# Kernel tuning notes

Measured on AMD Instinct MI355X. Metric: run time of the kernel, lower is better.

Reference implementation:

```python
import jax, jax.numpy as jnp
import numpy as np

GAMMA = 0.3          # surrogate gradient scale (LinearSpikeMC.gamma)
K = 2                # num_channels: multi-compartment count
T = 3                # timesteps
B = 4                # batch
LABELS = 10
CONV_CFG = [64, 64, 128, 128, 256, 256, 256, 512, 512, 512, 512, 512, 512]
POOL_AFTER = {1, 3, 6, 9}  # avg-pool after these conv indices (VGG16 'A' positions)


@jax.custom_vjp
def spike_mc(even, odd):
    # one-hot multi-compartment spike: fire where even>0 AND odd>=0
    return jnp.where((even > 0.0) & (odd >= 0.0), 1.0, 0.0).astype(even.dtype)

def _spike_fwd(even, odd):
    return spike_mc(even, odd), (even, odd)

def _spike_bwd(res, g):
    even, odd = res
    ge = GAMMA * jnp.maximum(1.0 - jnp.abs(even), 0.0) * g
    go = -GAMMA * jnp.maximum(1.0 - jnp.abs(odd), 0.0) * g
    # torch backward loop never writes the last odd compartment's grad
    go = go.at[-1].set(0.0)
    return ge, go

spike_mc.defvjp(_spike_fwd, _spike_bwd)


def conv3x3(x, w):
    return jax.lax.conv_general_dilated(
        x, w, (1, 1), 'SAME', dimension_numbers=('NCHW', 'OIHW', 'NCHW'))


def avgpool2(x):
    b, c, h, w = x.shape
    return x.reshape(b, c, h // 2, 2, w // 2, 2).mean(axis=(3, 5))


def lif(mem, syn, thr, leak):
    # leaky integrate; compartment i fires when 2^i*thr < mem <= 2^{i+1}*thr
    mem = leak * mem + syn
    pw = (2.0 ** jnp.arange(K, dtype=mem.dtype)).reshape((K,) + (1,) * mem.ndim)
    even = mem[None] / (pw * thr) - 1.0
    odd = 1.0 - mem[None] / (2.0 * pw * thr)
    sp = spike_mc(even, odd)            # [K, ...] one-hot spikes
    val = jnp.sum(pw * sp, axis=0)      # decoded value sum_i 2^i * s_i
    mem = mem - thr * val               # soft reset (reset_to_zero=0)
    return mem, val


def setup_inputs():
    key = jax.random.key(0)
    ks = jax.random.split(key, 32)
    inp = {"x": jax.random.normal(ks[0], (B, 3, 32, 32), jnp.float32)}
    in_c = 3
    for i, out_c in enumerate(CONV_CFG):
        std = float(np.sqrt(2.0 / (9.0 * out_c)))  # kaiming init from _initialize_weights2
        inp[f"w{i}"] = jax.random.normal(ks[1 + i], (out_c, in_c, 3, 3), jnp.float32) * std
        in_c = out_c
    inp["fc0"] = jax.random.normal(ks[20], (4096, 512 * 2 * 2), jnp.float32) * 0.01
    inp["fc1"] = jax.random.normal(ks[21], (4096, 4096), jnp.float32) * 0.01
    inp["fc2"] = jax.random.normal(ks[22], (LABELS, 4096), jnp.float32) * 0.01
    inp["thr"] = jnp.ones((15,), jnp.float32)   # per-layer thresholds
    inp["leak"] = jnp.ones((15,), jnp.float32)  # per-layer leaks
    return inp


def reference(x, w0, w1, w2, w3, w4, w5, w6, w7, w8, w9, w10, w11, w12,
              fc0, fc1, fc2, thr, leak):
    conv_ws = [w0, w1, w2, w3, w4, w5, w6, w7, w8, w9, w10, w11, w12]
    b = x.shape[0]
    # membranes sized at each conv's output resolution (neuron_init)
    mems = []
    s = 32
    for i, c in enumerate(CONV_CFG):
        mems.append(jnp.zeros((b, c, s, s), x.dtype))
        if i in POOL_AFTER:
            s //= 2
    carry0 = (tuple(mems),
              jnp.zeros((b, 4096), x.dtype),
              jnp.zeros((b, 4096), x.dtype),
              jnp.zeros((b, fc2.shape[0]), x.dtype))

    def step(carry, _):
        mems_c, m0, m1, logits = carry
        out = x  # analog input each timestep (input_encoding=1)
        new = []
        for i in range(13):
            m, out = lif(mems_c[i], conv3x3(out, conv_ws[i]), thr[i], leak[i])
            new.append(m)
            if i in POOL_AFTER:
                out = avgpool2(out)
        out = out.reshape(b, -1)
        m0, out = lif(m0, out @ fc0.T, thr[13], leak[13])
        m1, out = lif(m1, out @ fc1.T, thr[14], leak[14])
        logits = logits + out @ fc2.T  # final linear accumulates, no spiking
        return (tuple(new), m0, m1, logits), None

    carry, _ = jax.lax.scan(step, carry0, None, length=T)
    return carry[3]
```

## Files before the change

kernel.cpp:

```cpp
#include <hip/hip_runtime.h>


#define BATCH 4

__device__ __forceinline__ float lif_update(float mem_in, float syn, float thr,
                                            float leak, float* mem_out) {
    float m = leak * mem_in + syn;
    float val = 0.f;
    if ((m / thr - 1.f > 0.f) && (1.f - m / (2.f * thr) >= 0.f)) val += 1.f;
    if ((m / (2.f * thr) - 1.f > 0.f) && (1.f - m / (4.f * thr) >= 0.f)) val += 2.f;
    *mem_out = m - thr * val;
    return val;
}

__global__ void conv_lif0_kernel(const float* __restrict__ in,
                                 const float* __restrict__ w,
                                 float* __restrict__ out0,
                                 float* __restrict__ out1,
                                 float* __restrict__ out2,
                                 const float* __restrict__ thr_v,
                                 const float* __restrict__ leak_v,
                                 int IC, int OC, int H, int W, int n) {
    int idx = blockIdx.x * blockDim.x + threadIdx.x;
    if (idx >= n) return;
    int x  = idx % W;
    int y  = (idx / W) % H;
    int oc = (idx / (W * H)) % OC;
    int b  = idx / (W * H * OC);

    const float* wp = w + (size_t)oc * IC * 9;
    const float* ip = in + (size_t)b * IC * H * W;

    float syn = 0.f;
    for (int ic = 0; ic < IC; ++ic) {
        const float* ipc = ip + (size_t)ic * H * W;
        const float* wpc = wp + ic * 9;
#pragma unroll
        for (int ky = 0; ky < 3; ++ky) {
            int yy = y + ky - 1;
            if (yy < 0 || yy >= H) continue;
#pragma unroll
            for (int kx = 0; kx < 3; ++kx) {
                int xx = x + kx - 1;
                if (xx < 0 || xx >= W) continue;
                syn = fmaf(ipc[yy * W + xx], wpc[ky * 3 + kx], syn);
            }
        }
    }
    float thr = thr_v[0], leak = leak_v[0];
    float m = 0.f;
    float v0 = lif_update(m, syn, thr, leak, &m);
    float v1 = lif_update(m, syn, thr, leak, &m);
    float v2 = lif_update(m, syn, thr, leak, &m);
    out0[idx] = v0;
    out1[idx] = v1;
    out2[idx] = v2;
}

__device__ __forceinline__ void mid_load(float v[9], const float* __restrict__ ip,
                                         const int off[9], const bool msk[9]) {
#pragma unroll
    for (int k = 0; k < 9; ++k) v[k] = msk[k] ? ip[off[k]] : 0.f;
}

template <int OCT>
__device__ __forceinline__ void mid_fma(const float v[9], const float* __restrict__ wp,
                                        int IC, float acc[OCT]) {
#pragma unroll
    for (int t = 0; t < OCT; ++t) {
        const float* wt = wp + (size_t)t * IC * 9;
#pragma unroll
        for (int k = 0; k < 9; ++k) acc[t] = fmaf(v[k], wt[k], acc[t]);
    }
}

template <int OCT, int NW, int POOL>
__global__ __launch_bounds__(NW * 64)
void conv_mid3_kernel(const float* __restrict__ in0,
                      const float* __restrict__ in1,
                      const float* __restrict__ in2,
                      const float* __restrict__ w,
                      float* __restrict__ out0,
                      float* __restrict__ out1,
                      float* __restrict__ out2,
                      const float* __restrict__ thr_v,
                      const float* __restrict__ leak_v,
                      int layer, int IC, int OC, int H, int W) {
    int tid = threadIdx.x;
    int lane = tid & 63;
    int wv = tid >> 6;
    int ocg = OC / OCT;
    int HW = H * W;
    int chunks = HW >> 6;
    int bid = blockIdx.x;
    int g  = bid % ocg;
    int ch = (bid / ocg) % chunks;
    int b  = bid / (ocg * chunks);
    int rpw = 64 / W;
    int y = ch * rpw + lane / W;
    int x = lane % W;
    int oc0 = g * OCT;

    int off[9];
    bool msk[9];
#pragma unroll
    for (int ky = 0; ky < 3; ++ky)
#pragma unroll
        for (int kx = 0; kx < 3; ++kx) {
            int yy = y + ky - 1, xx = x + kx - 1;
            bool v = (yy >= 0 && yy < H && xx >= 0 && xx < W);
            msk[ky * 3 + kx] = v;
            off[ky * 3 + kx] = v ? yy * W + xx : 0;
        }

    size_t boff = (size_t)b * IC * HW;
    const float* ib[3] = {in0 + boff, in1 + boff, in2 + boff};
    float* const outs[3] = {out0, out1, out2};
    const float* wbase = w + (size_t)oc0 * IC * 9;

    float acc[3][OCT];
#pragma unroll
    for (int t = 0; t < 3; ++t)
#pragma unroll
        for (int q = 0; q < OCT; ++q) acc[t][q] = 0.f;

    int icpw = IC / NW;
    int ic0 = wv * icpw;
    int icend = ic0 + icpw;

    float vc[3][9];
#pragma unroll
    for (int t = 0; t < 3; ++t) mid_load(vc[t], ib[t] + (size_t)ic0 * HW, off, msk);

    for (int ic = ic0; ic < icend; ++ic) {
        int icn = (ic + 1 < icend) ? ic + 1 : ic;
        const float* wp = wbase + (size_t)ic * 9;
        float nv[3][9];
#pragma unroll
        for (int t = 0; t < 3; ++t) {
            mid_load(nv[t], ib[t] + (size_t)icn * HW, off, msk);
            mid_fma<OCT>(vc[t], wp, IC, acc[t]);
        }
#pragma unroll
        for (int t = 0; t < 3; ++t)
#pragma unroll
            for (int k = 0; k < 9; ++k) vc[t][k] = nv[t][k];
    }

    __shared__ float red[NW][OCT][64];
    __shared__ float vals[OCT][64];
    float thr = thr_v[layer], leak = leak_v[layer];
    float mem_reg = 0.f;
    int eq = tid >> 6, ep = tid & 63;
    int Wo = W >> 1, Ho = H >> 1;

#pragma unroll
    for (int t = 0; t < 3; ++t) {
        __syncthreads();
#pragma unroll
        for (int q = 0; q < OCT; ++q) red[wv][q][lane] = acc[t][q];
        __syncthreads();
        if (tid < OCT * 64) {
            float sum = 0.f;
#pragma unroll
            for (int q = 0; q < NW; ++q) sum += red[q][eq][ep];
            float val = lif_update(mem_reg, sum, thr, leak, &mem_reg);
            if (POOL) {
                vals[eq][ep] = val;
            } else {
                size_t idx = (size_t)(b * OC + oc0 + eq) * HW + ch * 64 + ep;
                outs[t][idx] = val;
            }
        }
        if (POOL) {
            __syncthreads();
            if (tid < OCT * 16) {
                int q = tid >> 4, s = tid & 15;
                int pr = s / Wo, pc = s % Wo;
                float pv = 0.25f * (vals[q][(2 * pr) * W + 2 * pc] +
                                    vals[q][(2 * pr) * W + 2 * pc + 1] +
                                    vals[q][(2 * pr + 1) * W + 2 * pc] +
                                    vals[q][(2 * pr + 1) * W + 2 * pc + 1]);
                size_t pidx = ((size_t)(b * OC + oc0 + q) * Ho +
                               (ch * (rpw >> 1) + pr)) * Wo + pc;
                outs[t][pidx] = pv;
            }
        }
    }
}

template <int S, int NW, int POOL>
__global__ __launch_bounds__(NW * 64)
void conv_small4_3_kernel(const float* __restrict__ in0,
                          const float* __restrict__ in1,
                          const float* __restrict__ in2,
                          const float* __restrict__ w,
                          float* __restrict__ out0,
                          float* __restrict__ out1,
                          float* __restrict__ out2,
                          const float* __restrict__ thr_v,
                          const float* __restrict__ leak_v,
                          int layer, int IC, int OC) {
    constexpr int SS = S * S;
    constexpr int M = 4 * SS;
    constexpr int LOG2M = (S == 4) ? 6 : 4;
    int tid = threadIdx.x;
    int lane = tid & 63;
    int wv = tid >> 6;
    int oc = blockIdx.x;

    const float* const ins[3] = {in0, in1, in2};
    float* const outs[3] = {out0, out1, out2};
    const float* wrow = w + (size_t)oc * IC * 9;

    __shared__ float red[NW][M];
    __shared__ float pvs[M];
    float thr = thr_v[layer], leak = leak_v[layer];
    float mem_reg = 0.f;

#pragma unroll
    for (int t = 0; t < 3; ++t) {
        const float* inb = ins[t];
        float acc[M];
#pragma unroll
        for (int i = 0; i < M; ++i) acc[i] = 0.f;

        for (int ic = lane + (wv << 6); ic < IC; ic += NW * 64) {
            const float* wp = wrow + (size_t)ic * 9;
            float wvv[9];
#pragma unroll
            for (int k = 0; k < 9; ++k) wvv[k] = wp[k];
#pragma unroll
            for (int b = 0; b < 4; ++b) {
                const float4* ip = (const float4*)(inb + (size_t)(b * IC + ic) * SS);
                float pv[SS];
#pragma unroll
                for (int q = 0; q < SS / 4; ++q) {
                    float4 t4 = ip[q];
                    pv[4 * q + 0] = t4.x;
                    pv[4 * q + 1] = t4.y;
                    pv[4 * q + 2] = t4.z;
                    pv[4 * q + 3] = t4.w;
                }
#pragma unroll
                for (int y = 0; y < S; ++y)
#pragma unroll
                    for (int x = 0; x < S; ++x) {
                        float a = acc[b * SS + y * S + x];
#pragma unroll
                        for (int ky = 0; ky < 3; ++ky) {
                            int yy = y + ky - 1;
                            if (yy < 0 || yy >= S) continue;
#pragma unroll
                            for (int kx = 0; kx < 3; ++kx) {
                                int xx = x + kx - 1;
                                if (xx < 0 || xx >= S) continue;
                                a = fmaf(pv[yy * S + xx], wvv[ky * 3 + kx], a);
                            }
                        }
                        acc[b * SS + y * S + x] = a;
                    }
            }
        }

#pragma unroll
        for (int step = 0; step < LOG2M; ++step) {
            const int offx = 1 << step;
            const int half = M >> (step + 1);
            const bool hi = (lane & offx) != 0;
#pragma unroll
            for (int i = 0; i < half; ++i) {
                float sent = hi ? acc[i] : acc[i + half];
                float got = __shfl_xor(sent, offx);
                acc[i] = (hi ? acc[i + half] : acc[i]) + got;
            }
        }
        float sum = acc[0];
#pragma unroll
        for (int offx = M; offx < 64; offx <<= 1) sum += __shfl_xor(sum, offx);

        __syncthreads();
        int o = (int)(__brev((unsigned)(lane & (M - 1))) >> (32 - LOG2M));
        if (lane < M) red[wv][o] = sum;
        __syncthreads();

        if (tid < M) {
            float tot = 0.f;
#pragma unroll
            for (int q = 0; q < NW; ++q) tot += red[q][tid];
            int b = tid / SS, p = tid % SS;
            float val = lif_update(mem_reg, tot, thr, leak, &mem_reg);
            if (POOL) {
                pvs[tid] = val;
            } else {
                size_t idx = (size_t)(b * OC + oc) * SS + p;
                outs[t][idx] = val;
            }
        }
        if (POOL) {
            __syncthreads();
            constexpr int Sh = S / 2, SSh = Sh * Sh;
            if (tid < 4 * SSh) {
                int b = tid / SSh, q = tid % SSh;
                int pr = q / Sh, pc = q % Sh;
                float pv = 0.25f * (pvs[b * SS + (2 * pr) * S + 2 * pc] +
                                    pvs[b * SS + (2 * pr) * S + 2 * pc + 1] +
                                    pvs[b * SS + (2 * pr + 1) * S + 2 * pc] +
                                    pvs[b * SS + (2 * pr + 1) * S + 2 * pc + 1]);
                outs[t][((size_t)(b * OC + oc) * Sh + pr) * Sh + pc] = pv;
            }
        }
    }
}

__global__ void fc_lif3_kernel(const float* __restrict__ in0,
                               const float* __restrict__ in1,
                               const float* __restrict__ in2,
                               const float* __restrict__ w,
                               float* __restrict__ out0,
                               float* __restrict__ out1,
                               float* __restrict__ out2,
                               const float* __restrict__ thr_v,
                               const float* __restrict__ leak_v,
                               int layer, int Kd, int N) {
    int wave = (blockIdx.x * blockDim.x + threadIdx.x) >> 6;
    int lane = threadIdx.x & 63;
    if (wave >= N) return;
    int j = wave;
    int K4 = Kd >> 2;
    const float4* wp = (const float4*)(w + (size_t)j * Kd);
    const float4* ip[3] = {(const float4*)in0, (const float4*)in1, (const float4*)in2};
    float* const outs[3] = {out0, out1, out2};

    float a[3][4];
#pragma unroll
    for (int t = 0; t < 3; ++t)
#pragma unroll
        for (int b = 0; b < 4; ++b) a[t][b] = 0.f;

    for (int k = lane; k < K4; k += 64) {
        float4 wv = wp[k];
#pragma unroll
        for (int t = 0; t < 3; ++t)
#pragma unroll
            for (int b = 0; b < 4; ++b) {
                float4 v = ip[t][b * K4 + k];
                a[t][b] = fmaf(wv.x, v.x, fmaf(wv.y, v.y,
                          fmaf(wv.z, v.z, fmaf(wv.w, v.w, a[t][b]))));
            }
    }
#pragma unroll
    for (int t = 0; t < 3; ++t)
#pragma unroll
        for (int b = 0; b < 4; ++b)
#pragma unroll
            for (int off = 32; off > 0; off >>= 1)
                a[t][b] += __shfl_xor(a[t][b], off);

    if (lane == 0) {
        float thr = thr_v[layer], leak = leak_v[layer];
#pragma unroll
        for (int b = 0; b < BATCH; ++b) {
            float m = 0.f;
#pragma unroll
            for (int t = 0; t < 3; ++t) {
                float val = lif_update(m, a[t][b], thr, leak, &m);
                outs[t][(size_t)b * N + j] = val;
            }
        }
    }
}

__global__ void fc2_acc3_kernel(const float* __restrict__ in0,
                                const float* __restrict__ in1,
                                const float* __restrict__ in2,
                                const float* __restrict__ w,
                                float* __restrict__ logits,
                                int Kd, int L) {
    int o = blockIdx.x;
    int l = o % L;
    int b = o / L;
    int K4 = Kd >> 2;
    const float4* ip[3] = {(const float4*)(in0 + (size_t)b * Kd),
                           (const float4*)(in1 + (size_t)b * Kd),
                           (const float4*)(in2 + (size_t)b * Kd)};
    const float4* wp = (const float4*)(w + (size_t)l * Kd);
    float st[3] = {0.f, 0.f, 0.f};
    for (int k = threadIdx.x; k < K4; k += 64) {
        float4 wv = wp[k];
#pragma unroll
        for (int t = 0; t < 3; ++t) {
            float4 iv = ip[t][k];
            st[t] = fmaf(iv.x, wv.x, fmaf(iv.y, wv.y,
                    fmaf(iv.z, wv.z, fmaf(iv.w, wv.w, st[t]))));
        }
    }
#pragma unroll
    for (int t = 0; t < 3; ++t)
#pragma unroll
        for (int off = 32; off > 0; off >>= 1) st[t] += __shfl_xor(st[t], off);
    if (threadIdx.x == 0) logits[o] = (st[0] + st[1]) + st[2];
}

extern "C" void kernel_launch(void* const* d_in, const int* in_sizes, int n_in,
                              void* d_out, int out_size, void* d_ws, size_t ws_size,
                              hipStream_t stream) {
    const float* x = (const float*)d_in[0];
    const float* convw[13];
    for (int i = 0; i < 13; ++i) convw[i] = (const float*)d_in[1 + i];
    const float* fc0 = (const float*)d_in[14];
    const float* fc1 = (const float*)d_in[15];
    const float* fc2 = (const float*)d_in[16];
    const float* thr = (const float*)d_in[17];
    const float* leak = (const float*)d_in[18];

    static const int IC[13] = {3, 64, 64, 128, 128, 256, 256, 256, 512, 512, 512, 512, 512};
    static const int OC[13] = {64, 64, 128, 128, 256, 256, 256, 512, 512, 512, 512, 512, 512};
    static const int HH[13] = {32, 32, 16, 16, 8, 8, 8, 4, 4, 4, 2, 2, 2};

    float* ws = (float*)d_ws;
    float* A[3];
    float* B[3];
    size_t off = 0;
    for (int i = 0; i < 3; ++i) { A[i] = ws + off; off += 262144; }
    for (int i = 0; i < 3; ++i) { B[i] = ws + off; off += 262144; }

    {
        int n = BATCH * 64 * 32 * 32;
        conv_lif0_kernel<<<(n + 255) / 256, 256, 0, stream>>>(
            x, convw[0], A[0], A[1], A[2], thr, leak, 3, 64, 32, 32, n);
    }

    float** src = A;
    float** dst = B;

    for (int i = 1; i <= 6; ++i) {
        int H = HH[i], W = HH[i];
        int blocks;
        if (i <= 3) {
            blocks = BATCH * (H * W / 64) * (OC[i] / 4);
            if (i == 1)
                conv_mid3_kernel<4, 8, 1><<<blocks, 512, 0, stream>>>(
                    src[0], src[1], src[2], convw[i], dst[0], dst[1], dst[2],
                    thr, leak, i, IC[i], OC[i], H, W);
            else if (i == 2)
                conv_mid3_kernel<4, 8, 0><<<blocks, 512, 0, stream>>>(
                    src[0], src[1], src[2], convw[i], dst[0], dst[1], dst[2],
                    thr, leak, i, IC[i], OC[i], H, W);
            else
                conv_mid3_kernel<4, 8, 1><<<blocks, 512, 0, stream>>>(
                    src[0], src[1], src[2], convw[i], dst[0], dst[1], dst[2],
                    thr, leak, i, IC[i], OC[i], H, W);
        } else {
            blocks = BATCH * (H * W / 64) * (OC[i] / 2);
            if (i == 6)
                conv_mid3_kernel<2, 8, 1><<<blocks, 512, 0, stream>>>(
                    src[0], src[1], src[2], convw[i], dst[0], dst[1], dst[2],
                    thr, leak, i, IC[i], OC[i], H, W);
            else
                conv_mid3_kernel<2, 8, 0><<<blocks, 512, 0, stream>>>(
                    src[0], src[1], src[2], convw[i], dst[0], dst[1], dst[2],
                    thr, leak, i, IC[i], OC[i], H, W);
        }
        float** tmp = src; src = dst; dst = tmp;
    }

    for (int i = 7; i <= 12; ++i) {
        if (i == 7)
            conv_small4_3_kernel<4, 4, 0><<<OC[i], 256, 0, stream>>>(
                src[0], src[1], src[2], convw[i], dst[0], dst[1], dst[2],
                thr, leak, i, IC[i], OC[i]);
        else if (i == 8)
            conv_small4_3_kernel<4, 8, 0><<<OC[i], 512, 0, stream>>>(
                src[0], src[1], src[2], convw[i], dst[0], dst[1], dst[2],
                thr, leak, i, IC[i], OC[i]);
        else if (i == 9)
            conv_small4_3_kernel<4, 8, 1><<<OC[i], 512, 0, stream>>>(
                src[0], src[1], src[2], convw[i], dst[0], dst[1], dst[2],
                thr, leak, i, IC[i], OC[i]);
        else
            conv_small4_3_kernel<2, 8, 0><<<OC[i], 512, 0, stream>>>(
                src[0], src[1], src[2], convw[i], dst[0], dst[1], dst[2],
                thr, leak, i, IC[i], OC[i]);
        float** tmp = src; src = dst; dst = tmp;
    }

    fc_lif3_kernel<<<(4096 * 64) / 256, 256, 0, stream>>>(
        src[0], src[1], src[2], fc0, dst[0], dst[1], dst[2],
        thr, leak, 13, 2048, 4096);
    { float** tmp = src; src = dst; dst = tmp; }

    fc_lif3_kernel<<<(4096 * 64) / 256, 256, 0, stream>>>(
        src[0], src[1], src[2], fc1, dst[0], dst[1], dst[2],
        thr, leak, 14, 4096, 4096);
    { float** tmp = src; src = dst; dst = tmp; }

    fc2_acc3_kernel<<<BATCH * 10, 64, 0, stream>>>(
        src[0], src[1], src[2], fc2, (float*)d_out, 4096, 10);
}
```

Measured before the change: 671.7 us.

## Stage halo input tiles in double-buffered shared memory for mid conv layers

The mid-layer conv kernel now cooperatively loads each input-channel round's 3x3 halo tiles for all three timesteps into double-buffered LDS. Each lane then reads its 9 taps from shared memory instead of issuing 9 masked global loads per timestep per channel. Width is made a template constant and weights are preloaded into registers per round. The cost is an extra __syncthreads per channel round and more shared memory, which may lower occupancy.

```diff
diff --git a/kernel.cpp b/kernel.cpp
--- a/kernel.cpp
+++ b/kernel.cpp
@@ -57,24 +57,36 @@
     out2[idx] = v2;
 }
 
-__device__ __forceinline__ void mid_load(float v[9], const float* __restrict__ ip,
-                                         const int off[9], const bool msk[9]) {
-#pragma unroll
-    for (int k = 0; k < 9; ++k) v[k] = msk[k] ? ip[off[k]] : 0.f;
-}
-
-template <int OCT>
-__device__ __forceinline__ void mid_fma(const float v[9], const float* __restrict__ wp,
-                                        int IC, float acc[OCT]) {
-#pragma unroll
-    for (int t = 0; t < OCT; ++t) {
-        const float* wt = wp + (size_t)t * IC * 9;
-#pragma unroll
-        for (int k = 0; k < 9; ++k) acc[t] = fmaf(v[k], wt[k], acc[t]);
-    }
-}
-
-template <int OCT, int NW, int POOL>
+template <int NW, int W_>
+__device__ __forceinline__ void stage_tiles(float* __restrict__ dst, int tid,
+                                            int rnd, int icpw, int y0,
+                                            const float* __restrict__ i0,
+                                            const float* __restrict__ i1,
+                                            const float* __restrict__ i2) {
+    constexpr int TWD = W_ + 2;
+    constexpr int TH = 64 / W_ + 2;
+    constexpr int TILE = TH * TWD;
+    constexpr int HW = W_ * W_;
+    constexpr int TOT = NW * 3 * TILE;
+    for (int s = tid; s < TOT; s += NW * 64) {
+        int icg = s / (3 * TILE);
+        int rem = s - icg * 3 * TILE;
+        int t = rem / TILE;
+        int p = rem - t * TILE;
+        int r = p / TWD;
+        int c = p - r * TWD;
+        int ic = icg * icpw + rnd;
+        int gy = y0 + r - 1;
+        int gx = c - 1;
+        const float* pt = (t == 0) ? i0 : ((t == 1) ? i1 : i2);
+        float val = 0.f;
+        if (gy >= 0 && gy < W_ && gx >= 0 && gx < W_)
+            val = pt[(size_t)ic * HW + gy * W_ + gx];
+        dst[s] = val;
+    }
+}
+
+template <int OCT, int NW, int POOL, int W_>
 __global__ __launch_bounds__(NW * 64)
 void conv_mid3_kernel(const float* __restrict__ in0,
                       const float* __restrict__ in1,
@@ -85,66 +97,80 @@
                       float* __restrict__ out2,
                       const float* __restrict__ thr_v,
                       const float* __restrict__ leak_v,
-                      int layer, int IC, int OC, int H, int W) {
+                      int layer, int IC, int OC) {
+    constexpr int HW = W_ * W_;
+    constexpr int RPW = 64 / W_;
+    constexpr int TH = RPW + 2;
+    constexpr int TWD = W_ + 2;
+    constexpr int TILE = TH * TWD;
+    constexpr int CHUNKS = HW / 64;
+
     int tid = threadIdx.x;
     int lane = tid & 63;
     int wv = tid >> 6;
     int ocg = OC / OCT;
-    int HW = H * W;
-    int chunks = HW >> 6;
     int bid = blockIdx.x;
     int g  = bid % ocg;
-    int ch = (bid / ocg) % chunks;
-    int b  = bid / (ocg * chunks);
-    int rpw = 64 / W;
-    int y = ch * rpw + lane / W;
-    int x = lane % W;
+    int ch = (bid / ocg) % CHUNKS;
+    int b  = bid / (ocg * CHUNKS);
+    int y0 = ch * RPW;
     int oc0 = g * OCT;
 
-    int off[9];
-    bool msk[9];
-#pragma unroll
-    for (int ky = 0; ky < 3; ++ky)
-#pragma unroll
-        for (int kx = 0; kx < 3; ++kx) {
-            int yy = y + ky - 1, xx = x + kx - 1;
-            bool v = (yy >= 0 && yy < H && xx >= 0 && xx < W);
-            msk[ky * 3 + kx] = v;
-            off[ky * 3 + kx] = v ? yy * W + xx : 0;
-        }
-
     size_t boff = (size_t)b * IC * HW;
-    const float* ib[3] = {in0 + boff, in1 + boff, in2 + boff};
+    const float* i0 = in0 + boff;
+    const float* i1 = in1 + boff;
+    const float* i2 = in2 + boff;
     float* const outs[3] = {out0, out1, out2};
     const float* wbase = w + (size_t)oc0 * IC * 9;
 
+    int icpw = IC / NW;
+
+    __shared__ float stage[2][NW * 3 * TILE];
+
     float acc[3][OCT];
 #pragma unroll
     for (int t = 0; t < 3; ++t)
 #pragma unroll
         for (int q = 0; q < OCT; ++q) acc[t][q] = 0.f;
 
-    int icpw = IC / NW;
-    int ic0 = wv * icpw;
-    int icend = ic0 + icpw;
-
-    float vc[3][9];
-#pragma unroll
-    for (int t = 0; t < 3; ++t) mid_load(vc[t], ib[t] + (size_t)ic0 * HW, off, msk);
-
-    for (int ic = ic0; ic < icend; ++ic) {
-        int icn = (ic + 1 < icend) ? ic + 1 : ic;
+    int r0 = lane / W_;
+    int c0 = lane % W_;
+
+    stage_tiles<NW, W_>(stage[0], tid, 0, icpw, y0, i0, i1, i2);
+    __syncthreads();
+
+    for (int rnd = 0; rnd < icpw; ++rnd) {
+        int buf = rnd & 1;
+        if (rnd + 1 < icpw)
+            stage_tiles<NW, W_>(stage[buf ^ 1], tid, rnd + 1, icpw, y0, i0, i1, i2);
+
+        int ic = wv * icpw + rnd;
         const float* wp = wbase + (size_t)ic * 9;
-        float nv[3][9];
+        float wvv[OCT][9];
+#pragma unroll
+        for (int q = 0; q < OCT; ++q) {
+            const float* wq = wp + (size_t)q * IC * 9;
+#pragma unroll
+            for (int k = 0; k < 9; ++k) wvv[q][k] = wq[k];
+        }
+
+        const float* sb = stage[buf] + wv * (3 * TILE);
 #pragma unroll
         for (int t = 0; t < 3; ++t) {
-            mid_load(nv[t], ib[t] + (size_t)icn * HW, off, msk);
-            mid_fma<OCT>(vc[t], wp, IC, acc[t]);
-        }
-#pragma unroll
-        for (int t = 0; t < 3; ++t)
-#pragma unroll
-            for (int k = 0; k < 9; ++k) vc[t][k] = nv[t][k];
+            const float* tp = sb + t * TILE + r0 * TWD + c0;
+            float tv[9];
+#pragma unroll
+            for (int ky = 0; ky < 3; ++ky)
+#pragma unroll
+                for (int kx = 0; kx < 3; ++kx)
+                    tv[ky * 3 + kx] = tp[ky * TWD + kx];
+#pragma unroll
+            for (int q = 0; q < OCT; ++q)
+#pragma unroll
+                for (int k = 0; k < 9; ++k)
+                    acc[t][q] = fmaf(tv[k], wvv[q][k], acc[t][q]);
+        }
+        __syncthreads();
     }
 
     __shared__ float red[NW][OCT][64];
@@ -152,7 +178,7 @@
     float thr = thr_v[layer], leak = leak_v[layer];
     float mem_reg = 0.f;
     int eq = tid >> 6, ep = tid & 63;
-    int Wo = W >> 1, Ho = H >> 1;
+    constexpr int Wo = W_ / 2, Ho = W_ / 2;
 
 #pragma unroll
     for (int t = 0; t < 3; ++t) {
@@ -177,12 +203,12 @@
             if (tid < OCT * 16) {
                 int q = tid >> 4, s = tid & 15;
                 int pr = s / Wo, pc = s % Wo;
-                float pv = 0.25f * (vals[q][(2 * pr) * W + 2 * pc] +
-                                    vals[q][(2 * pr) * W + 2 * pc + 1] +
-                                    vals[q][(2 * pr + 1) * W + 2 * pc] +
-                                    vals[q][(2 * pr + 1) * W + 2 * pc + 1]);
+                float pv = 0.25f * (vals[q][(2 * pr) * W_ + 2 * pc] +
+                                    vals[q][(2 * pr) * W_ + 2 * pc + 1] +
+                                    vals[q][(2 * pr + 1) * W_ + 2 * pc] +
+                                    vals[q][(2 * pr + 1) * W_ + 2 * pc + 1]);
                 size_t pidx = ((size_t)(b * OC + oc0 + q) * Ho +
-                               (ch * (rpw >> 1) + pr)) * Wo + pc;
+                               (ch * (RPW >> 1) + pr)) * Wo + pc;
                 outs[t][pidx] = pv;
             }
         }
@@ -416,7 +442,6 @@
 
     static const int IC[13] = {3, 64, 64, 128, 128, 256, 256, 256, 512, 512, 512, 512, 512};
     static const int OC[13] = {64, 64, 128, 128, 256, 256, 256, 512, 512, 512, 512, 512, 512};
-    static const int HH[13] = {32, 32, 16, 16, 8, 8, 8, 4, 4, 4, 2, 2, 2};
 
     float* ws = (float*)d_ws;
     float* A[3];
@@ -434,36 +459,35 @@
     float** src = A;
     float** dst = B;
 
-    for (int i = 1; i <= 6; ++i) {
-        int H = HH[i], W = HH[i];
-        int blocks;
-        if (i <= 3) {
-            blocks = BATCH * (H * W / 64) * (OC[i] / 4);
-            if (i == 1)
-                conv_mid3_kernel<4, 8, 1><<<blocks, 512, 0, stream>>>(
-                    src[0], src[1], src[2], convw[i], dst[0], dst[1], dst[2],
-                    thr, leak, i, IC[i], OC[i], H, W);
-            else if (i == 2)
-                conv_mid3_kernel<4, 8, 0><<<blocks, 512, 0, stream>>>(
-                    src[0], src[1], src[2], convw[i], dst[0], dst[1], dst[2],
-                    thr, leak, i, IC[i], OC[i], H, W);
-            else
-                conv_mid3_kernel<4, 8, 1><<<blocks, 512, 0, stream>>>(
-                    src[0], src[1], src[2], convw[i], dst[0], dst[1], dst[2],
-                    thr, leak, i, IC[i], OC[i], H, W);
-        } else {
-            blocks = BATCH * (H * W / 64) * (OC[i] / 2);
-            if (i == 6)
-                conv_mid3_kernel<2, 8, 1><<<blocks, 512, 0, stream>>>(
-                    src[0], src[1], src[2], convw[i], dst[0], dst[1], dst[2],
-                    thr, leak, i, IC[i], OC[i], H, W);
-            else
-                conv_mid3_kernel<2, 8, 0><<<blocks, 512, 0, stream>>>(
-                    src[0], src[1], src[2], convw[i], dst[0], dst[1], dst[2],
-                    thr, leak, i, IC[i], OC[i], H, W);
-        }
-        float** tmp = src; src = dst; dst = tmp;
-    }
+    conv_mid3_kernel<4, 8, 1, 32><<<BATCH * 16 * (OC[1] / 4), 512, 0, stream>>>(
+        src[0], src[1], src[2], convw[1], dst[0], dst[1], dst[2],
+        thr, leak, 1, IC[1], OC[1]);
+    { float** tmp = src; src = dst; dst = tmp; }
+
+    conv_mid3_kernel<4, 8, 0, 16><<<BATCH * 4 * (OC[2] / 4), 512, 0, stream>>>(
+        src[0], src[1], src[2], convw[2], dst[0], dst[1], dst[2],
+        thr, leak, 2, IC[2], OC[2]);
+    { float** tmp = src; src = dst; dst = tmp; }
+
+    conv_mid3_kernel<4, 8, 1, 16><<<BATCH * 4 * (OC[3] / 4), 512, 0, stream>>>(
+        src[0], src[1], src[2], convw[3], dst[0], dst[1], dst[2],
+        thr, leak, 3, IC[3], OC[3]);
+    { float** tmp = src; src = dst; dst = tmp; }
+
+    conv_mid3_kernel<2, 8, 0, 8><<<BATCH * (OC[4] / 2), 512, 0, stream>>>(
+        src[0], src[1], src[2], convw[4], dst[0], dst[1], dst[2],
+        thr, leak, 4, IC[4], OC[4]);
+    { float** tmp = src; src = dst; dst = tmp; }
+
+    conv_mid3_kernel<2, 8, 0, 8><<<BATCH * (OC[5] / 2), 512, 0, stream>>>(
+        src[0], src[1], src[2], convw[5], dst[0], dst[1], dst[2],
+        thr, leak, 5, IC[5], OC[5]);
+    { float** tmp = src; src = dst; dst = tmp; }
+
+    conv_mid3_kernel<2, 8, 1, 8><<<BATCH * (OC[6] / 2), 512, 0, stream>>>(
+        src[0], src[1], src[2], convw[6], dst[0], dst[1], dst[2],
+        thr, leak, 6, IC[6], OC[6]);
+    { float** tmp = src; src = dst; dst = tmp; }
 
     for (int i = 7; i <= 12; ++i) {
         if (i == 7)
```

Measured after the change: 773.3 us. +15.1%, slower.
